# Kernel tuning notes

Measured on AMD Instinct MI355X. Metric: run time of the kernel, lower is better.

Reference implementation:

```python
import jax, jax.numpy as jnp
import numpy as np

BETA = 0.25  # commitment cost
EPS = 1e-10


def _vq_layer(xf, cb):
    # xf: [M, D] flattened features, cb: [K, D] codebook
    K = cb.shape[0]
    M = xf.shape[0]
    d = (jnp.sum(xf * xf, axis=-1, keepdims=True)
         - 2.0 * (xf @ cb.T)
         + jnp.sum(cb * cb, axis=-1))
    idx = jnp.argmin(d, axis=-1)          # [M]
    q = cb[idx]                           # [M, D]
    # commitment + codebook loss (VQ-VAE)
    commit = jnp.mean((jax.lax.stop_gradient(q) - xf) ** 2)
    cbloss = jnp.mean((q - jax.lax.stop_gradient(xf)) ** 2)
    loss = cbloss + BETA * commit
    # straight-through estimator
    q_st = xf + jax.lax.stop_gradient(q - xf)
    # codebook usage perplexity
    counts = jnp.zeros((K,), dtype=xf.dtype).at[idx].add(1.0)
    p = counts / M
    perplexity = jnp.exp(-jnp.sum(p * jnp.log(p + EPS)))
    return q_st, idx, loss, perplexity


def setup_inputs() -> dict:
    key = jax.random.key(0)
    k1, k2 = jax.random.split(key)
    B, N, D, H, W, K = 32, 4, 128, 32, 32, 1024
    x = jax.random.normal(k1, (B, N * D, H, W), dtype=jnp.float32)
    codebooks = jax.random.normal(k2, (N, K, D), dtype=jnp.float32)
    return {"x": x, "codebooks": codebooks}


def reference(x, codebooks):
    B, C, H, W = x.shape
    N, K, D = codebooks.shape
    assert C == N * D
    M = B * H * W
    # [B, N*D, H, W] -> [N, M, D]
    xs = x.reshape(B, N, D, H, W).transpose(1, 0, 3, 4, 2).reshape(N, M, D)
    q, idx, loss, perp = jax.vmap(_vq_layer)(xs, codebooks)
    # quantized_cat: [N, M, D] -> [B, N*D, H, W]  (cat along channel dim)
    quantized_cat = (q.reshape(N, B, H, W, D)
                      .transpose(1, 0, 4, 2, 3)
                      .reshape(B, N * D, H, W))
    # indices_cat: [N, M] -> [B, N, H, W]
    indices_cat = idx.reshape(N, B, H, W).transpose(1, 0, 2, 3)
    return quantized_cat, indices_cat, loss, perp
```

## Files before the change

### kernel.cpp

```cpp
#include <hip/hip_runtime.h>

#define B_ 32
#define N_ 4
#define D_ 128
#define M_ 32768
#define K_ 1024

#define IDX_OFF 16777216
#define LOSS_OFF 16908288
#define PERP_OFF 16908292

#define WS_LOSS 0
#define WS_CNT 1024
#define WS_ENORM 8192
#define WS_BPACK_F 16384
#define BPACK_LAYER_US 131072

#define SBIAS 384.0f
#define MARGIN 0.04f

typedef _Float16 f16x8 __attribute__((ext_vector_type(8)));
typedef float f32x4 __attribute__((ext_vector_type(4)));

union FragH {
  f16x8 v;
  _Float16 h[8];
  ushort u16[8];
  uint4 q;
};

__device__ __forceinline__ void gload_lds16(const void* g, void* l) {
  __builtin_amdgcn_global_load_lds(
      (const __attribute__((address_space(1))) unsigned int*)g,
      (__attribute__((address_space(3))) unsigned int*)l, 16, 0, 0);
}

__global__ void vq_pack(const float* __restrict__ cb, float* __restrict__ ws) {
  int blk = blockIdx.x, tid = threadIdx.x;
  if (blk < 256) {
    int n = blk >> 6, tile = blk & 63;
    int s = tid >> 6, lane = tid & 63;
    int code = tile * 16 + (lane & 15);
    int dbase = s * 32 + ((lane >> 4) << 3);
    const float* src = cb + ((size_t)(n * K_ + code)) * D_ + dbase;
    float4 v0 = *(const float4*)src;
    float4 v1 = *(const float4*)(src + 4);
    float v[8] = {v0.x, v0.y, v0.z, v0.w, v1.x, v1.y, v1.z, v1.w};
    FragH f;
#pragma unroll
    for (int j = 0; j < 8; ++j) f.h[j] = (_Float16)v[j];
    ushort* base = (ushort*)(ws + WS_BPACK_F) + (size_t)n * BPACK_LAYER_US +
                   (size_t)(tile * 4 + s) * 512 + lane * 8;
    *(uint4*)base = f.q;
  } else if (blk < 1280) {
    int lane = tid & 63, w = tid >> 6;
    int waveid = (blk - 256) * 4 + w;
    int n = waveid >> 10, k = waveid & 1023;
    const float2* row = (const float2*)(cb + (size_t)(n * K_ + k) * D_);
    float2 v = row[lane];
    float ss = fmaf(v.x, v.x, v.y * v.y);
#pragma unroll
    for (int off = 32; off; off >>= 1) ss += __shfl_down(ss, off, 64);
    if (lane == 0) ws[WS_ENORM + n * K_ + k] = SBIAS - 0.5f * ss;
  } else {
#pragma unroll
    for (int i = 0; i < 20; ++i) ws[i * 256 + tid] = 0.f;
  }
}

__global__ __launch_bounds__(256, 4) void vq_main(const float* __restrict__ x,
                                                  const float* __restrict__ cb,
                                                  float* __restrict__ ws,
                                                  float* __restrict__ out) {
  __shared__ alignas(16) ushort Bsm[18432];
  const int tid = threadIdx.x;
  const int bid = blockIdx.x;
  const int n = bid >> 8;
  const int mblk = bid & 255;
  const int b = mblk >> 3;
  const int hw0 = (mblk & 7) << 7;

  const int lane = tid & 63, w = tid >> 6;
  const int quad = lane >> 4, l15 = lane & 15;

  const float* xbase = x + (size_t)((b * 4 + n) * 128) * 1024 + hw0;
  const float* cbn = cb + (size_t)n * K_ * D_;
  const float* enB = ws + WS_ENORM + n * K_;
  const ushort* bpack_n = (ushort*)(ws + WS_BPACK_F) + (size_t)n * BPACK_LAYER_US;

  char* ext = (char*)Bsm + 32768;
  int* sIdx = (int*)ext;
  float* dist = (float*)(ext + 512);
  int* list = (int*)(ext + 1024);
  int* lcnt = (int*)(ext + 1536);

  if (tid == 0) *lcnt = 0;

  f16x8 ah[2][4];
#pragma unroll
  for (int set = 0; set < 2; ++set) {
    const int hwl = w * 32 + set * 16 + l15;
    float xs = 0.f;
#pragma unroll
    for (int s = 0; s < 4; ++s) {
      const int dbase = s * 32 + quad * 8;
      FragH fh;
#pragma unroll
      for (int j = 0; j < 8; ++j) {
        float v = xbase[(size_t)(dbase + j) * 1024 + hwl];
        xs = fmaf(v, v, xs);
        fh.h[j] = (_Float16)v;
      }
      ah[set][s] = fh.v;
    }
    xs += __shfl_xor(xs, 16, 64);
    xs += __shfl_xor(xs, 32, 64);
    if (l15 == lane) dist[w * 32 + set * 16 + l15] = xs;
  }

  uint best[8], best2[8];
#pragma unroll
  for (int i = 0; i < 8; ++i) { best[i] = 0u; best2[i] = 0u; }

  const uint4* gsrc = (const uint4*)bpack_n;
  uint4* Bsm4 = (uint4*)Bsm;

#pragma unroll
  for (int i = 0; i < 4; ++i)
    gload_lds16(gsrc + i * 256 + w * 64 + lane, Bsm4 + i * 256 + w * 64);

#pragma unroll 1
  for (int c = 0; c < 16; ++c) {
    __syncthreads();
    if (c < 15) {
      const uint4* src = gsrc + (c + 1) * 1024;
      uint4* dst = Bsm4 + ((c + 1) & 1) * 1024;
#pragma unroll
      for (int i = 0; i < 4; ++i)
        gload_lds16(src + i * 256 + w * 64 + lane, dst + i * 256 + w * 64);
    }
    const ushort* Bcur = Bsm + (c & 1) * 8192;
#pragma unroll
    for (int tin = 0; tin < 4; ++tin) {
      const int t = c * 4 + tin;
      const uint tinv = (uint)(63 - t);
      float en = enB[t * 16 + l15];
      f16x8 bv[4];
#pragma unroll
      for (int s = 0; s < 4; ++s) {
        const ushort* p = Bcur + (tin * 4 + s) * 512 + lane * 8;
        bv[s] = ((const FragH*)p)->v;
      }
      f32x4 acc[2];
#pragma unroll
      for (int set = 0; set < 2; ++set) acc[set] = (f32x4){0.f, 0.f, 0.f, 0.f};
#pragma unroll
      for (int s = 0; s < 4; ++s) {
#pragma unroll
        for (int set = 0; set < 2; ++set)
          acc[set] = __builtin_amdgcn_mfma_f32_16x16x32_f16(ah[set][s], bv[s], acc[set], 0, 0, 0);
      }
#pragma unroll
      for (int set = 0; set < 2; ++set) {
#pragma unroll
        for (int r = 0; r < 4; ++r) {
          float sb = acc[set][r] + en;
          uint key = (__float_as_uint(sb) & 0xFFFFFFC0u) | tinv;
          uint ob = best[set * 4 + r];
          uint mn = key < ob ? key : ob;
          best[set * 4 + r] = key > ob ? key : ob;
          if (mn > best2[set * 4 + r]) best2[set * 4 + r] = mn;
        }
      }
    }
  }
  __syncthreads();

  uint* sS = (uint*)Bsm;
  uint* sS2 = (uint*)((char*)Bsm + 8704);
#pragma unroll
  for (int set = 0; set < 2; ++set) {
#pragma unroll
    for (int r = 0; r < 4; ++r) {
      int m = w * 32 + set * 16 + quad * 4 + r;
      sS[m * 17 + l15] = best[set * 4 + r];
      sS2[m * 17 + l15] = best2[set * 4 + r];
    }
  }
  __syncthreads();

  if (tid < 128) {
    int m = tid;
    uint g1 = 0, g2 = 0;
    int gi = 0;
#pragma unroll 4
    for (int li = 0; li < 16; ++li) {
      uint key = sS[m * 17 + li];
      uint sb = key >> 6;
      int kk = (int)(63u - (key & 63u)) * 16 + li;
      if (sb > g1) { g2 = g1; g1 = sb; gi = kk; }
      else {
        if (sb == g1 && kk < gi) gi = kk;
        if (sb > g2) g2 = sb;
      }
      uint sb2 = sS2[m * 17 + li] >> 6;
      if (sb2 > g2) g2 = sb2;
    }
    sIdx[m] = gi;
    float s1f = __uint_as_float(g1 << 6);
    dist[m] = dist[m] - 2.0f * (s1f - SBIAS);
    float gap = s1f - __uint_as_float(g2 << 6);
    if (gap < MARGIN) {
      int pos = atomicAdd(lcnt, 1);
      list[pos] = m;
    }
  }
  __syncthreads();

  const int cnt = *lcnt;
  if (cnt > 0) {
    char* rbase = (char*)Bsm;
    float* xrs = (float*)rbase;
    double* dred = (double*)(rbase + 2048);
    int* kred = (int*)(rbase + 3072);
    const int g = tid >> 3, h = tid & 7;
    for (int g0 = 0; g0 < cnt; g0 += 4) {
      const int R = (cnt - g0 < 4) ? (cnt - g0) : 4;
      for (int e = tid; e < R * 128; e += 256) {
        int r = e >> 7, d = e & 127;
        xrs[e] = xbase[(size_t)d * 1024 + list[g0 + r]];
      }
      __syncthreads();
      double pbd[4];
      int pbk[4];
#pragma unroll
      for (int r = 0; r < 4; ++r) { pbd[r] = 1e300; pbk[r] = 0; }
#pragma unroll 1
      for (int c = 0; c < 32; ++c) {
        const int k = c * 32 + g;
        const float4* er = (const float4*)(cbn + (size_t)k * D_) + h * 4;
        float4 E0 = er[0], E1 = er[1], E2 = er[2], E3 = er[3];
#pragma unroll
        for (int r = 0; r < 4; ++r) {
          if (r < R) {
            const float4* xp4 = (const float4*)(xrs + r * 128) + h * 4;
            double pd = 0.0;
            float4 xv;
            xv = xp4[0];
            { double d0=(double)xv.x-E0.x, d1=(double)xv.y-E0.y, d2=(double)xv.z-E0.z, d3=(double)xv.w-E0.w;
              pd=fma(d0,d0,pd); pd=fma(d1,d1,pd); pd=fma(d2,d2,pd); pd=fma(d3,d3,pd); }
            xv = xp4[1];
            { double d0=(double)xv.x-E1.x, d1=(double)xv.y-E1.y, d2=(double)xv.z-E1.z, d3=(double)xv.w-E1.w;
              pd=fma(d0,d0,pd); pd=fma(d1,d1,pd); pd=fma(d2,d2,pd); pd=fma(d3,d3,pd); }
            xv = xp4[2];
            { double d0=(double)xv.x-E2.x, d1=(double)xv.y-E2.y, d2=(double)xv.z-E2.z, d3=(double)xv.w-E2.w;
              pd=fma(d0,d0,pd); pd=fma(d1,d1,pd); pd=fma(d2,d2,pd); pd=fma(d3,d3,pd); }
            xv = xp4[3];
            { double d0=(double)xv.x-E3.x, d1=(double)xv.y-E3.y, d2=(double)xv.z-E3.z, d3=(double)xv.w-E3.w;
              pd=fma(d0,d0,pd); pd=fma(d1,d1,pd); pd=fma(d2,d2,pd); pd=fma(d3,d3,pd); }
            pd += __shfl_xor(pd, 1, 64);
            pd += __shfl_xor(pd, 2, 64);
            pd += __shfl_xor(pd, 4, 64);
            if (pd < pbd[r]) { pbd[r] = pd; pbk[r] = k; }
          }
        }
      }
      if (h == 0) {
#pragma unroll
        for (int r = 0; r < 4; ++r)
          if (r < R) { dred[r * 32 + g] = pbd[r]; kred[r * 32 + g] = pbk[r]; }
      }
      __syncthreads();
      if (tid < R) {
        double bd = 1e300;
        int bk = 0;
#pragma unroll 4
        for (int g2 = 0; g2 < 32; ++g2) {
          double d = dred[tid * 32 + g2];
          int kk = kred[tid * 32 + g2];
          if (d < bd || (d == bd && kk < bk)) { bd = d; bk = kk; }
        }
        int m = list[g0 + tid];
        sIdx[m] = bk;
        dist[m] = (float)bd;
      }
      __syncthreads();
    }
  }

  if (tid < 128) {
    int bi = sIdx[tid];
    out[IDX_OFF + (b * 4 + n) * 1024 + hw0 + tid] = (float)bi;
    atomicAdd(ws + WS_CNT + n * K_ + bi, 1.0f);
  }
  float lp = (tid < 128) ? dist[tid] : 0.f;
#pragma unroll
  for (int off = 32; off; off >>= 1) lp += __shfl_down(lp, off, 64);
  if (lane == 0 && w < 2) atomicAdd(ws + WS_LOSS + n, lp);
  __syncthreads();

  float* Qs = (float*)Bsm;
  float* out0 = out + (size_t)((b * 4 + n) * 128) * 1024 + hw0;
#pragma unroll 1
  for (int h = 0; h < 2; ++h) {
    const int m = tid & 127, part = tid >> 7;
    const float* src = cbn + (size_t)sIdx[m] * D_ + h * 64 + part * 32;
#pragma unroll
    for (int i = 0; i < 8; ++i) {
      float4 v = ((const float4*)src)[i];
      int dl = part * 32 + i * 4;
      Qs[(dl + 0) * 128 + m] = v.x;
      Qs[(dl + 1) * 128 + m] = v.y;
      Qs[(dl + 2) * 128 + m] = v.z;
      Qs[(dl + 3) * 128 + m] = v.w;
    }
    __syncthreads();
#pragma unroll
    for (int it = 0; it < 8; ++it) {
      int e = it * 256 + tid;
      int m4 = (e & 31) * 4;
      int dl = e >> 5;
      float4 v = *(float4*)(Qs + dl * 128 + m4);
      *(float4*)(out0 + (size_t)(h * 64 + dl) * 1024 + m4) = v;
    }
    __syncthreads();
  }
}

__global__ void vq_finalize(const float* __restrict__ ws, float* __restrict__ out) {
  int n = blockIdx.x;
  int t = threadIdx.x;
  const float* counts = ws + WS_CNT + n * K_;
  float s = 0.f;
  for (int k = t; k < K_; k += 256) {
    float p = counts[k] * (1.0f / 32768.0f);
    s += p * logf(p + 1e-10f);
  }
  __shared__ float red[4];
#pragma unroll
  for (int off = 32; off; off >>= 1) s += __shfl_down(s, off, 64);
  if ((t & 63) == 0) red[t >> 6] = s;
  __syncthreads();
  if (t == 0) {
    s = red[0] + red[1] + red[2] + red[3];
    out[PERP_OFF + n] = expf(-s);
    out[LOSS_OFF + n] = 1.25f * ws[WS_LOSS + n] / 4194304.0f;
  }
}

extern "C" void kernel_launch(void* const* d_in, const int* in_sizes, int n_in,
                              void* d_out, int out_size, void* d_ws, size_t ws_size,
                              hipStream_t stream) {
  const float* x = (const float*)d_in[0];
  const float* cb = (const float*)d_in[1];
  float* out = (float*)d_out;
  float* ws = (float*)d_ws;
  vq_pack<<<1281, 256, 0, stream>>>(cb, ws);
  vq_main<<<1024, 256, 0, stream>>>(x, cb, ws, out);
  vq_finalize<<<4, 256, 0, stream>>>(ws, out);
}
```

Before: 252.5 us.

## Double rows per block, fuse finalize via ticket, simplify argmin tracking

```diff
diff --git a/kernel.cpp b/kernel.cpp
--- a/kernel.cpp
+++ b/kernel.cpp
@@ -11,10 +11,12 @@
 #define PERP_OFF 16908292
 
 #define WS_LOSS 0
+#define WS_TICKET 4
 #define WS_CNT 1024
 #define WS_ENORM 8192
 #define WS_BPACK_F 16384
 #define BPACK_LAYER_US 131072
+#define WS_EN2D 278528
 
 #define SBIAS 384.0f
 #define MARGIN 0.04f
@@ -52,33 +54,39 @@
     ushort* base = (ushort*)(ws + WS_BPACK_F) + (size_t)n * BPACK_LAYER_US +
                    (size_t)(tile * 4 + s) * 512 + lane * 8;
     *(uint4*)base = f.q;
-  } else if (blk < 1280) {
+  } else if (blk < 512) {
     int lane = tid & 63, w = tid >> 6;
-    int waveid = (blk - 256) * 4 + w;
-    int n = waveid >> 10, k = waveid & 1023;
-    const float2* row = (const float2*)(cb + (size_t)(n * K_ + k) * D_);
-    float2 v = row[lane];
-    float ss = fmaf(v.x, v.x, v.y * v.y);
-#pragma unroll
-    for (int off = 32; off; off >>= 1) ss += __shfl_down(ss, off, 64);
-    if (lane == 0) ws[WS_ENORM + n * K_ + k] = SBIAS - 0.5f * ss;
+    int kg0 = (blk - 256) * 16 + w * 4;
+#pragma unroll 1
+    for (int cc = 0; cc < 4; ++cc) {
+      int kg = kg0 + cc;
+      const float2* row = (const float2*)(cb + (size_t)kg * D_);
+      float2 v = row[lane];
+      double sd = (double)v.x * (double)v.x + (double)v.y * (double)v.y;
+#pragma unroll
+      for (int off = 32; off; off >>= 1) sd += __shfl_down(sd, off, 64);
+      if (lane == 0) {
+        ws[WS_ENORM + kg] = SBIAS - 0.5f * (float)sd;
+        ((double*)(ws + WS_EN2D))[kg] = sd;
+      }
+    }
   } else {
 #pragma unroll
     for (int i = 0; i < 20; ++i) ws[i * 256 + tid] = 0.f;
   }
 }
 
-__global__ __launch_bounds__(256, 4) void vq_main(const float* __restrict__ x,
+__global__ __launch_bounds__(256, 2) void vq_main(const float* __restrict__ x,
                                                   const float* __restrict__ cb,
                                                   float* __restrict__ ws,
                                                   float* __restrict__ out) {
-  __shared__ alignas(16) ushort Bsm[18432];
+  __shared__ alignas(16) char Lds[38944];
   const int tid = threadIdx.x;
   const int bid = blockIdx.x;
-  const int n = bid >> 8;
-  const int mblk = bid & 255;
-  const int b = mblk >> 3;
-  const int hw0 = (mblk & 7) << 7;
+  const int n = bid >> 7;
+  const int mblk = bid & 127;
+  const int b = mblk >> 2;
+  const int hw0 = (mblk & 3) << 8;
 
   const int lane = tid & 63, w = tid >> 6;
   const int quad = lane >> 4, l15 = lane & 15;
@@ -88,18 +96,26 @@
   const float* enB = ws + WS_ENORM + n * K_;
   const ushort* bpack_n = (ushort*)(ws + WS_BPACK_F) + (size_t)n * BPACK_LAYER_US;
 
-  char* ext = (char*)Bsm + 32768;
-  int* sIdx = (int*)ext;
-  float* dist = (float*)(ext + 512);
-  int* list = (int*)(ext + 1024);
-  int* lcnt = (int*)(ext + 1536);
+  int* sIdx = (int*)(Lds + 34816);
+  float* dist = (float*)(Lds + 35840);
+  float* xn = (float*)(Lds + 36864);
+  int* list = (int*)(Lds + 37888);
+  int* lcnt = (int*)(Lds + 38912);
+  float* red = (float*)(Lds + 38920);
 
   if (tid == 0) *lcnt = 0;
 
-  f16x8 ah[2][4];
-#pragma unroll
-  for (int set = 0; set < 2; ++set) {
-    const int hwl = w * 32 + set * 16 + l15;
+  const uint4* gsrc = (const uint4*)bpack_n;
+  uint4* Bsm4 = (uint4*)Lds;
+
+#pragma unroll
+  for (int i = 0; i < 4; ++i)
+    gload_lds16(gsrc + i * 256 + w * 64 + lane, Bsm4 + i * 256 + w * 64);
+
+  f16x8 ah[4][4];
+#pragma unroll
+  for (int set = 0; set < 4; ++set) {
+    const int hwl = w * 64 + set * 16 + l15;
     float xs = 0.f;
 #pragma unroll
     for (int s = 0; s < 4; ++s) {
@@ -115,19 +131,12 @@
     }
     xs += __shfl_xor(xs, 16, 64);
     xs += __shfl_xor(xs, 32, 64);
-    if (l15 == lane) dist[w * 32 + set * 16 + l15] = xs;
-  }
-
-  uint best[8], best2[8];
-#pragma unroll
-  for (int i = 0; i < 8; ++i) { best[i] = 0u; best2[i] = 0u; }
-
-  const uint4* gsrc = (const uint4*)bpack_n;
-  uint4* Bsm4 = (uint4*)Bsm;
-
-#pragma unroll
-  for (int i = 0; i < 4; ++i)
-    gload_lds16(gsrc + i * 256 + w * 64 + lane, Bsm4 + i * 256 + w * 64);
+    if (quad == 0) xn[w * 64 + set * 16 + l15] = xs;
+  }
+
+  float best[16], best2[16];
+#pragma unroll
+  for (int i = 0; i < 16; ++i) { best[i] = 0.f; best2[i] = 0.f; }
 
 #pragma unroll 1
   for (int c = 0; c < 16; ++c) {
@@ -139,7 +148,7 @@
       for (int i = 0; i < 4; ++i)
         gload_lds16(src + i * 256 + w * 64 + lane, dst + i * 256 + w * 64);
     }
-    const ushort* Bcur = Bsm + (c & 1) * 8192;
+    const ushort* Bcur = (const ushort*)Lds + (c & 1) * 8192;
 #pragma unroll
     for (int tin = 0; tin < 4; ++tin) {
       const int t = c * 4 + tin;
@@ -151,46 +160,44 @@
         const ushort* p = Bcur + (tin * 4 + s) * 512 + lane * 8;
         bv[s] = ((const FragH*)p)->v;
       }
-      f32x4 acc[2];
-#pragma unroll
-      for (int set = 0; set < 2; ++set) acc[set] = (f32x4){0.f, 0.f, 0.f, 0.f};
+      f32x4 acc[4];
+#pragma unroll
+      for (int set = 0; set < 4; ++set) acc[set] = (f32x4){en, en, en, en};
 #pragma unroll
       for (int s = 0; s < 4; ++s) {
 #pragma unroll
-        for (int set = 0; set < 2; ++set)
+        for (int set = 0; set < 4; ++set)
           acc[set] = __builtin_amdgcn_mfma_f32_16x16x32_f16(ah[set][s], bv[s], acc[set], 0, 0, 0);
       }
 #pragma unroll
-      for (int set = 0; set < 2; ++set) {
+      for (int set = 0; set < 4; ++set) {
 #pragma unroll
         for (int r = 0; r < 4; ++r) {
-          float sb = acc[set][r] + en;
-          uint key = (__float_as_uint(sb) & 0xFFFFFFC0u) | tinv;
-          uint ob = best[set * 4 + r];
-          uint mn = key < ob ? key : ob;
-          best[set * 4 + r] = key > ob ? key : ob;
-          if (mn > best2[set * 4 + r]) best2[set * 4 + r] = mn;
+          float key = __uint_as_float((__float_as_uint(acc[set][r]) & 0xFFFFFFC0u) | tinv);
+          float ob = best[set * 4 + r];
+          best[set * 4 + r] = fmaxf(key, ob);
+          best2[set * 4 + r] = __builtin_amdgcn_fmed3f(key, ob, best2[set * 4 + r]);
         }
       }
     }
   }
   __syncthreads();
 
-  uint* sS = (uint*)Bsm;
-  uint* sS2 = (uint*)((char*)Bsm + 8704);
-#pragma unroll
-  for (int set = 0; set < 2; ++set) {
+  uint* sS = (uint*)Lds;
+  uint* sS2 = (uint*)(Lds + 17408);
+#pragma unroll
+  for (int set = 0; set < 4; ++set) {
 #pragma unroll
     for (int r = 0; r < 4; ++r) {
-      int m = w * 32 + set * 16 + quad * 4 + r;
-      sS[m * 17 + l15] = best[set * 4 + r];
-      sS2[m * 17 + l15] = best2[set * 4 + r];
-    }
-  }
-  __syncthreads();
-
-  if (tid < 128) {
-    int m = tid;
+      int m = w * 64 + set * 16 + quad * 4 + r;
+      sS[m * 17 + l15] = __float_as_uint(best[set * 4 + r]);
+      sS2[m * 17 + l15] = __float_as_uint(best2[set * 4 + r]);
+    }
+  }
+  __syncthreads();
+
+  {
+    const int m = tid;
     uint g1 = 0, g2 = 0;
     int gi = 0;
 #pragma unroll 4
@@ -208,7 +215,7 @@
     }
     sIdx[m] = gi;
     float s1f = __uint_as_float(g1 << 6);
-    dist[m] = dist[m] - 2.0f * (s1f - SBIAS);
+    dist[m] = xn[m] - 2.0f * (s1f - SBIAS);
     float gap = s1f - __uint_as_float(g2 << 6);
     if (gap < MARGIN) {
       int pos = atomicAdd(lcnt, 1);
@@ -219,17 +226,15 @@
 
   const int cnt = *lcnt;
   if (cnt > 0) {
-    char* rbase = (char*)Bsm;
-    float* xrs = (float*)rbase;
-    double* dred = (double*)(rbase + 2048);
-    int* kred = (int*)(rbase + 3072);
+    float* xrs = (float*)Lds;
+    double* dred = (double*)(Lds + 2048);
+    int* kred = (int*)(Lds + 3072);
+    const double* en2 = (const double*)(ws + WS_EN2D) + n * K_;
     const int g = tid >> 3, h = tid & 7;
     for (int g0 = 0; g0 < cnt; g0 += 4) {
       const int R = (cnt - g0 < 4) ? (cnt - g0) : 4;
-      for (int e = tid; e < R * 128; e += 256) {
-        int r = e >> 7, d = e & 127;
-        xrs[e] = xbase[(size_t)d * 1024 + list[g0 + r]];
-      }
+      for (int e = tid; e < R * 128; e += 256)
+        xrs[e] = xbase[(size_t)(e & 127) * 1024 + list[g0 + (e >> 7)]];
       __syncthreads();
       double pbd[4];
       int pbk[4];
@@ -240,28 +245,30 @@
         const int k = c * 32 + g;
         const float4* er = (const float4*)(cbn + (size_t)k * D_) + h * 4;
         float4 E0 = er[0], E1 = er[1], E2 = er[2], E3 = er[3];
+        double e2 = en2[k];
 #pragma unroll
         for (int r = 0; r < 4; ++r) {
           if (r < R) {
             const float4* xp4 = (const float4*)(xrs + r * 128) + h * 4;
-            double pd = 0.0;
+            double dot = 0.0;
             float4 xv;
             xv = xp4[0];
-            { double d0=(double)xv.x-E0.x, d1=(double)xv.y-E0.y, d2=(double)xv.z-E0.z, d3=(double)xv.w-E0.w;
-              pd=fma(d0,d0,pd); pd=fma(d1,d1,pd); pd=fma(d2,d2,pd); pd=fma(d3,d3,pd); }
+            dot = fma((double)xv.x, (double)E0.x, dot); dot = fma((double)xv.y, (double)E0.y, dot);
+            dot = fma((double)xv.z, (double)E0.z, dot); dot = fma((double)xv.w, (double)E0.w, dot);
             xv = xp4[1];
-            { double d0=(double)xv.x-E1.x, d1=(double)xv.y-E1.y, d2=(double)xv.z-E1.z, d3=(double)xv.w-E1.w;
-              pd=fma(d0,d0,pd); pd=fma(d1,d1,pd); pd=fma(d2,d2,pd); pd=fma(d3,d3,pd); }
+            dot = fma((double)xv.x, (double)E1.x, dot); dot = fma((double)xv.y, (double)E1.y, dot);
+            dot = fma((double)xv.z, (double)E1.z, dot); dot = fma((double)xv.w, (double)E1.w, dot);
             xv = xp4[2];
-            { double d0=(double)xv.x-E2.x, d1=(double)xv.y-E2.y, d2=(double)xv.z-E2.z, d3=(double)xv.w-E2.w;
-              pd=fma(d0,d0,pd); pd=fma(d1,d1,pd); pd=fma(d2,d2,pd); pd=fma(d3,d3,pd); }
+            dot = fma((double)xv.x, (double)E2.x, dot); dot = fma((double)xv.y, (double)E2.y, dot);
+            dot = fma((double)xv.z, (double)E2.z, dot); dot = fma((double)xv.w, (double)E2.w, dot);
             xv = xp4[3];
-            { double d0=(double)xv.x-E3.x, d1=(double)xv.y-E3.y, d2=(double)xv.z-E3.z, d3=(double)xv.w-E3.w;
-              pd=fma(d0,d0,pd); pd=fma(d1,d1,pd); pd=fma(d2,d2,pd); pd=fma(d3,d3,pd); }
-            pd += __shfl_xor(pd, 1, 64);
-            pd += __shfl_xor(pd, 2, 64);
-            pd += __shfl_xor(pd, 4, 64);
-            if (pd < pbd[r]) { pbd[r] = pd; pbk[r] = k; }
+            dot = fma((double)xv.x, (double)E3.x, dot); dot = fma((double)xv.y, (double)E3.y, dot);
+            dot = fma((double)xv.z, (double)E3.z, dot); dot = fma((double)xv.w, (double)E3.w, dot);
+            dot += __shfl_xor(dot, 1, 64);
+            dot += __shfl_xor(dot, 2, 64);
+            dot += __shfl_xor(dot, 4, 64);
+            double v = e2 - 2.0 * dot;
+            if (v < pbd[r]) { pbd[r] = v; pbk[r] = k; }
           }
         }
       }
@@ -275,76 +282,79 @@
         double bd = 1e300;
         int bk = 0;
 #pragma unroll 4
-        for (int g2 = 0; g2 < 32; ++g2) {
-          double d = dred[tid * 32 + g2];
-          int kk = kred[tid * 32 + g2];
+        for (int g2i = 0; g2i < 32; ++g2i) {
+          double d = dred[tid * 32 + g2i];
+          int kk = kred[tid * 32 + g2i];
           if (d < bd || (d == bd && kk < bk)) { bd = d; bk = kk; }
         }
         int m = list[g0 + tid];
         sIdx[m] = bk;
-        dist[m] = (float)bd;
+        dist[m] = xn[m] + (float)bd;
       }
       __syncthreads();
     }
   }
 
-  if (tid < 128) {
+  {
     int bi = sIdx[tid];
     out[IDX_OFF + (b * 4 + n) * 1024 + hw0 + tid] = (float)bi;
     atomicAdd(ws + WS_CNT + n * K_ + bi, 1.0f);
-  }
-  float lp = (tid < 128) ? dist[tid] : 0.f;
-#pragma unroll
-  for (int off = 32; off; off >>= 1) lp += __shfl_down(lp, off, 64);
-  if (lane == 0 && w < 2) atomicAdd(ws + WS_LOSS + n, lp);
-  __syncthreads();
-
-  float* Qs = (float*)Bsm;
+    float lp = dist[tid];
+#pragma unroll
+    for (int off = 32; off; off >>= 1) lp += __shfl_down(lp, off, 64);
+    if (lane == 0) atomicAdd(ws + WS_LOSS + n, lp);
+  }
+  __syncthreads();
+
+  float* Qs = (float*)Lds;
   float* out0 = out + (size_t)((b * 4 + n) * 128) * 1024 + hw0;
 #pragma unroll 1
-  for (int h = 0; h < 2; ++h) {
-    const int m = tid & 127, part = tid >> 7;
-    const float* src = cbn + (size_t)sIdx[m] * D_ + h * 64 + part * 32;
+  for (int h = 0; h < 4; ++h) {
+    const float* src = cbn + (size_t)sIdx[tid] * D_ + h * 32;
 #pragma unroll
     for (int i = 0; i < 8; ++i) {
       float4 v = ((const float4*)src)[i];
-      int dl = part * 32 + i * 4;
-      Qs[(dl + 0) * 128 + m] = v.x;
-      Qs[(dl + 1) * 128 + m] = v.y;
-      Qs[(dl + 2) * 128 + m] = v.z;
-      Qs[(dl + 3) * 128 + m] = v.w;
+      int dl = i * 4;
+      Qs[(dl + 0) * 256 + tid] = v.x;
+      Qs[(dl + 1) * 256 + tid] = v.y;
+      Qs[(dl + 2) * 256 + tid] = v.z;
+      Qs[(dl + 3) * 256 + tid] = v.w;
     }
     __syncthreads();
 #pragma unroll
     for (int it = 0; it < 8; ++it) {
       int e = it * 256 + tid;
-      int m4 = (e & 31) * 4;
-      int dl = e >> 5;
-      float4 v = *(float4*)(Qs + dl * 128 + m4);
-      *(float4*)(out0 + (size_t)(h * 64 + dl) * 1024 + m4) = v;
+      int dl = e >> 6;
+      int m4 = (e & 63) * 4;
+      float4 v = *(float4*)(Qs + dl * 256 + m4);
+      *(float4*)(out0 + (size_t)(h * 32 + dl) * 1024 + m4) = v;
     }
     __syncthreads();
   }
-}
-
-__global__ void vq_finalize(const float* __restrict__ ws, float* __restrict__ out) {
-  int n = blockIdx.x;
-  int t = threadIdx.x;
-  const float* counts = ws + WS_CNT + n * K_;
-  float s = 0.f;
-  for (int k = t; k < K_; k += 256) {
-    float p = counts[k] * (1.0f / 32768.0f);
-    s += p * logf(p + 1e-10f);
-  }
-  __shared__ float red[4];
-#pragma unroll
-  for (int off = 32; off; off >>= 1) s += __shfl_down(s, off, 64);
-  if ((t & 63) == 0) red[t >> 6] = s;
-  __syncthreads();
-  if (t == 0) {
-    s = red[0] + red[1] + red[2] + red[3];
-    out[PERP_OFF + n] = expf(-s);
-    out[LOSS_OFF + n] = 1.25f * ws[WS_LOSS + n] / 4194304.0f;
+
+  __threadfence();
+  if (tid == 0) {
+    int tk = atomicAdd((int*)ws + WS_TICKET + n, 1);
+    *lcnt = (tk == 127) ? 1 : 0;
+  }
+  __syncthreads();
+  if (*lcnt) {
+    float s = 0.f;
+    for (int k = tid; k < K_; k += 256) {
+      float c = atomicAdd(ws + WS_CNT + n * K_ + k, 0.0f);
+      float p = c * (1.0f / 32768.0f);
+      s += p * logf(p + 1e-10f);
+    }
+#pragma unroll
+    for (int off = 32; off; off >>= 1) s += __shfl_down(s, off, 64);
+    if ((tid & 63) == 0) red[tid >> 6] = s;
+    __syncthreads();
+    if (tid == 0) {
+      s = red[0] + red[1] + red[2] + red[3];
+      out[PERP_OFF + n] = expf(-s);
+      float L = atomicAdd(ws + WS_LOSS + n, 0.0f);
+      out[LOSS_OFF + n] = 1.25f * L / 4194304.0f;
+    }
   }
 }
 
@@ -355,7 +365,6 @@
   const float* cb = (const float*)d_in[1];
   float* out = (float*)d_out;
   float* ws = (float*)d_ws;
-  vq_pack<<<1281, 256, 0, stream>>>(cb, ws);
-  vq_main<<<1024, 256, 0, stream>>>(x, cb, ws, out);
-  vq_finalize<<<4, 256, 0, stream>>>(ws, out);
+  vq_pack<<<513, 256, 0, stream>>>(cb, ws);
+  vq_main<<<512, 256, 0, stream>>>(x, cb, ws, out);
 }
```

Measured after the change: 296.4 us. 17.4% more time.
